# Performance work log

Measured on AMD Instinct MI355X. Metric: run time of the kernel, lower is better.

## Reference

```python
import jax, jax.numpy as jnp
import numpy as np

B, T, C, A, H = 2048, 2048, 8, 27, 8  # batch, timesteps, conv in-channels, n attrs, hidden nodes
KEEP = 0.9  # dropout rate 0.1


def setup_inputs() -> dict:
    key = jax.random.key(0)
    ks = jax.random.split(key, 10)
    uni = lambda k, s: jax.random.uniform(k, s, jnp.float32, -0.05, 0.05)  # keras RandomUniform default
    # inverted dropout masks (values 0 or 1/keep); the original reuses the same seed
    # for both attrs dropouts and the same seed for both hidden dropouts -> shared masks
    mask_attrs = jax.random.bernoulli(ks[8], KEEP, (B, A)).astype(jnp.float32) / KEEP
    mask_hidden = jax.random.bernoulli(ks[9], KEEP, (B, H)).astype(jnp.float32) / KEEP
    return {
        "x": jax.random.normal(ks[0], (B, T, C), jnp.float32),
        "attrs": jax.random.normal(ks[1], (B, A), jnp.float32),
        "c2_weight_w1": uni(ks[2], (A, H)),
        "c2_weight_b1": jnp.zeros((H,), jnp.float32),
        "c2_weight_w2": uni(ks[3], (H, C)),
        "c2_weight_b2": jnp.zeros((C,), jnp.float32),
        "c2_bias_w1": uni(ks[4], (A, H)),
        "c2_bias_b1": jnp.zeros((H,), jnp.float32),
        "c2_bias_w2": uni(ks[5], (H, 1)),
        "c2_bias_b2": jnp.zeros((1,), jnp.float32),
        "mask_attrs": mask_attrs,
        "mask_hidden": mask_hidden,
    }


def reference(x, attrs, c2_weight_w1, c2_weight_b1, c2_weight_w2, c2_weight_b2,
              c2_bias_w1, c2_bias_b1, c2_bias_w2, c2_bias_b2,
              mask_attrs, mask_hidden):
    a = attrs * mask_attrs  # [B, A] shared dropout (same seed in both branches)
    # per-sample conv kernel (kernel_size=1, so just a [B, C] vector)
    hw = jax.nn.relu(a @ c2_weight_w1 + c2_weight_b1) * mask_hidden  # [B, H]
    kernel = jnp.tanh(hw @ c2_weight_w2 + c2_weight_b2)              # [B, C]
    # per-sample bias
    hb = jax.nn.relu(a @ c2_bias_w1 + c2_bias_b1) * mask_hidden      # [B, H]
    bias = jnp.tanh(hb @ c2_bias_w2 + c2_bias_b2)                    # [B, 1]
    # kernel-size-1 valid conv == per-sample channel contraction, batched across B
    y = jnp.einsum('btc,bc->bt', x, kernel) + bias                   # [B, T]
    return jax.nn.elu(y)[..., None]                                  # [B, T, 1]
```

## Files before the change

kernel.cpp:

```cpp
#include <hip/hip_runtime.h>

#define BB 2048
#define TT 2048
#define CC 8
#define AA 27
#define HH 8

__global__ __launch_bounds__(256) void regional_conv2(
    const float* __restrict__ x,
    const float* __restrict__ attrs,
    const float* __restrict__ w1,
    const float* __restrict__ b1,
    const float* __restrict__ w2,
    const float* __restrict__ b2,
    const float* __restrict__ bw1,
    const float* __restrict__ bb1,
    const float* __restrict__ bw2,
    const float* __restrict__ bb2,
    const float* __restrict__ mask_attrs,
    const float* __restrict__ mask_hidden,
    float* __restrict__ out)
{
    const int idx = blockIdx.x * 256 + threadIdx.x;
    const int b   = idx >> 11;

    const float4* xp = reinterpret_cast<const float4*>(x + (size_t)idx * CC);
    const float4 x0 = xp[0];
    const float4 x1 = xp[1];

    __shared__ float s_h[2 * HH];
    __shared__ float s_ker[CC];
    __shared__ float s_bias;

    const int tid = threadIdx.x;

    if (tid < HH) {
        float hw = b1[tid];
        float hb = bb1[tid];
        const float* ab = attrs      + b * AA;
        const float* mb = mask_attrs + b * AA;
        #pragma unroll
        for (int i = 0; i < AA; ++i) {
            const float a = ab[i] * mb[i];
            hw = fmaf(a, w1 [i * HH + tid], hw);
            hb = fmaf(a, bw1[i * HH + tid], hb);
        }
        const float mh = mask_hidden[b * HH + tid];
        s_h[tid]      = fmaxf(hw, 0.0f) * mh;
        s_h[HH + tid] = fmaxf(hb, 0.0f) * mh;
    }
    __syncthreads();

    if (tid < CC) {
        float acc = b2[tid];
        #pragma unroll
        for (int j = 0; j < HH; ++j)
            acc = fmaf(s_h[j], w2[j * CC + tid], acc);
        s_ker[tid] = tanhf(acc);
        if (tid == 0) {
            float accb = bb2[0];
            #pragma unroll
            for (int j = 0; j < HH; ++j)
                accb = fmaf(s_h[HH + j], bw2[j], accb);
            s_bias = tanhf(accb);
        }
    }
    __syncthreads();

    float y = s_bias;
    y = fmaf(x0.x, s_ker[0], y);
    y = fmaf(x0.y, s_ker[1], y);
    y = fmaf(x0.z, s_ker[2], y);
    y = fmaf(x0.w, s_ker[3], y);
    y = fmaf(x1.x, s_ker[4], y);
    y = fmaf(x1.y, s_ker[5], y);
    y = fmaf(x1.z, s_ker[6], y);
    y = fmaf(x1.w, s_ker[7], y);
    out[idx] = (y > 0.0f) ? y : expm1f(y);
}

extern "C" void kernel_launch(void* const* d_in, const int* in_sizes, int n_in,
                              void* d_out, int out_size, void* d_ws, size_t ws_size,
                              hipStream_t stream) {
    const float* x    = (const float*)d_in[0];
    const float* at   = (const float*)d_in[1];
    const float* w1   = (const float*)d_in[2];
    const float* b1   = (const float*)d_in[3];
    const float* w2   = (const float*)d_in[4];
    const float* b2   = (const float*)d_in[5];
    const float* bw1  = (const float*)d_in[6];
    const float* bb1  = (const float*)d_in[7];
    const float* bw2  = (const float*)d_in[8];
    const float* bb2  = (const float*)d_in[9];
    const float* ma   = (const float*)d_in[10];
    const float* mh   = (const float*)d_in[11];
    float* out = (float*)d_out;

    const int total  = BB * TT;
    const int blocks = total / 256;
    regional_conv2<<<blocks, 256, 0, stream>>>(
        x, at, w1, b1, w2, b2, bw1, bb1, bw2, bb2, ma, mh, out);
}
```

Measured before the change: 240.3 us.

## Split per-sample MLP into a separate kernel ahead of the streaming conv

Moves the per-sample MLP that builds the kernel and bias vectors into a small precomputation kernel that writes them to workspace. The main streaming kernel then just loads 9 floats per sample, with no shared memory, barriers or serial MLP per block. Previously each of 16384 blocks recomputed the MLP for its sample with only 8 threads active while the rest waited at barriers. The trade-off is an extra kernel launch and a dependency through global memory.

```diff
diff --git a/kernel.cpp b/kernel.cpp
--- a/kernel.cpp
+++ b/kernel.cpp
@@ -6,8 +6,7 @@
 #define AA 27
 #define HH 8
 
-__global__ __launch_bounds__(256) void regional_conv2(
-    const float* __restrict__ x,
+__global__ __launch_bounds__(256) void mlp_kernel(
     const float* __restrict__ attrs,
     const float* __restrict__ w1,
     const float* __restrict__ b1,
@@ -19,6 +18,55 @@
     const float* __restrict__ bb2,
     const float* __restrict__ mask_attrs,
     const float* __restrict__ mask_hidden,
+    float* __restrict__ ker,
+    float* __restrict__ bias)
+{
+    const int tid = threadIdx.x;
+    const int s   = tid >> 3;
+    const int h   = tid & 7;
+    const int b   = blockIdx.x * 32 + s;
+
+    __shared__ float s_hw[32][HH];
+    __shared__ float s_hb[32][HH];
+
+    {
+        float hw = b1[h];
+        float hb = bb1[h];
+        const float* ab = attrs      + b * AA;
+        const float* mb = mask_attrs + b * AA;
+        #pragma unroll
+        for (int i = 0; i < AA; ++i) {
+            const float a = ab[i] * mb[i];
+            hw = fmaf(a, w1 [i * HH + h], hw);
+            hb = fmaf(a, bw1[i * HH + h], hb);
+        }
+        const float mh = mask_hidden[b * HH + h];
+        s_hw[s][h] = fmaxf(hw, 0.0f) * mh;
+        s_hb[s][h] = fmaxf(hb, 0.0f) * mh;
+    }
+    __syncthreads();
+
+    {
+        const int c = h;
+        float acc = b2[c];
+        #pragma unroll
+        for (int j = 0; j < HH; ++j)
+            acc = fmaf(s_hw[s][j], w2[j * CC + c], acc);
+        ker[b * CC + c] = tanhf(acc);
+        if (c == 0) {
+            float accb = bb2[0];
+            #pragma unroll
+            for (int j = 0; j < HH; ++j)
+                accb = fmaf(s_hb[s][j], bw2[j], accb);
+            bias[b] = tanhf(accb);
+        }
+    }
+}
+
+__global__ __launch_bounds__(256) void stream_kernel(
+    const float* __restrict__ x,
+    const float* __restrict__ ker,
+    const float* __restrict__ bias,
     float* __restrict__ out)
 {
     const int idx = blockIdx.x * 256 + threadIdx.x;
@@ -28,54 +76,19 @@
     const float4 x0 = xp[0];
     const float4 x1 = xp[1];
 
-    __shared__ float s_h[2 * HH];
-    __shared__ float s_ker[CC];
-    __shared__ float s_bias;
+    const float4* kp = reinterpret_cast<const float4*>(ker + b * CC);
+    const float4 k0 = kp[0];
+    const float4 k1 = kp[1];
+    float y = bias[b];
 
-    const int tid = threadIdx.x;
-
-    if (tid < HH) {
-        float hw = b1[tid];
-        float hb = bb1[tid];
-        const float* ab = attrs      + b * AA;
-        const float* mb = mask_attrs + b * AA;
-        #pragma unroll
-        for (int i = 0; i < AA; ++i) {
-            const float a = ab[i] * mb[i];
-            hw = fmaf(a, w1 [i * HH + tid], hw);
-            hb = fmaf(a, bw1[i * HH + tid], hb);
-        }
-        const float mh = mask_hidden[b * HH + tid];
-        s_h[tid]      = fmaxf(hw, 0.0f) * mh;
-        s_h[HH + tid] = fmaxf(hb, 0.0f) * mh;
-    }
-    __syncthreads();
-
-    if (tid < CC) {
-        float acc = b2[tid];
-        #pragma unroll
-        for (int j = 0; j < HH; ++j)
-            acc = fmaf(s_h[j], w2[j * CC + tid], acc);
-        s_ker[tid] = tanhf(acc);
-        if (tid == 0) {
-            float accb = bb2[0];
-            #pragma unroll
-            for (int j = 0; j < HH; ++j)
-                accb = fmaf(s_h[HH + j], bw2[j], accb);
-            s_bias = tanhf(accb);
-        }
-    }
-    __syncthreads();
-
-    float y = s_bias;
-    y = fmaf(x0.x, s_ker[0], y);
-    y = fmaf(x0.y, s_ker[1], y);
-    y = fmaf(x0.z, s_ker[2], y);
-    y = fmaf(x0.w, s_ker[3], y);
-    y = fmaf(x1.x, s_ker[4], y);
-    y = fmaf(x1.y, s_ker[5], y);
-    y = fmaf(x1.z, s_ker[6], y);
-    y = fmaf(x1.w, s_ker[7], y);
+    y = fmaf(x0.x, k0.x, y);
+    y = fmaf(x0.y, k0.y, y);
+    y = fmaf(x0.z, k0.z, y);
+    y = fmaf(x0.w, k0.w, y);
+    y = fmaf(x1.x, k1.x, y);
+    y = fmaf(x1.y, k1.y, y);
+    y = fmaf(x1.z, k1.z, y);
+    y = fmaf(x1.w, k1.w, y);
     out[idx] = (y > 0.0f) ? y : expm1f(y);
 }
 
@@ -96,8 +109,12 @@
     const float* mh   = (const float*)d_in[11];
     float* out = (float*)d_out;
 
+    float* ker  = (float*)d_ws;
+    float* bias = (float*)d_ws + BB * CC;
+
+    mlp_kernel<<<BB / 32, 256, 0, stream>>>(
+        at, w1, b1, w2, b2, bw1, bb1, bw2, bb2, ma, mh, ker, bias);
+
     const int total  = BB * TT;
-    const int blocks = total / 256;
-    regional_conv2<<<blocks, 256, 0, stream>>>(
-        x, at, w1, b1, w2, b2, bw1, bb1, bw2, bb2, ma, mh, out);
+    stream_kernel<<<total / 256, 256, 0, stream>>>(x, ker, bias, out);
 }
```

Result: faster. 215.2 us (-10.4%).
